# Kernel optimization log

Measured on AMD Instinct MI355X. Metric: run time of the kernel, lower is better.

Reference implementation:

```python
import jax, jax.numpy as jnp
import numpy as np

NB, B, L, D, H = 4, 4, 1024, 512, 8
E = D // H  # head dim = 64
SCALE = 1.0 / np.sqrt(E)


def setup_inputs() -> dict:
    key = jax.random.key(0)
    ks = jax.random.split(key, 18)
    w = lambda k, shape: (jax.random.normal(k, shape, dtype=jnp.float32) * 0.02)
    inp = {
        'x': jax.random.normal(ks[0], (NB, B, L, D), dtype=jnp.float32),
        # per-block intra-attention projections, stored [in, out] (x @ W + b)
        'Wq': w(ks[1], (NB, D, D)), 'bq': w(ks[2], (NB, D)),
        'Wk': w(ks[3], (NB, D, D)), 'bk': w(ks[4], (NB, D)),
        'Wv': w(ks[5], (NB, D, D)), 'bv': w(ks[6], (NB, D)),
        'Wo': w(ks[7], (NB, D, D)), 'bo': w(ks[8], (NB, D)),
        # shared inter (router) attention projections
        'iWq': w(ks[9], (D, D)), 'ibq': w(ks[10], (D,)),
        'iWk': w(ks[11], (D, D)), 'ibk': w(ks[12], (D,)),
        'iWv': w(ks[13], (D, D)), 'ibv': w(ks[14], (D,)),
        'iWo': w(ks[15], (D, D)), 'ibo': w(ks[16], (D,)),
    }
    return inp


def _full_attn(q, k, v):
    # q,k,v: [..., S, H, E] with batch dims leading; unmasked FullAttention
    scores = jnp.einsum('...lhe,...she->...hls', q, k) * SCALE
    A = jax.nn.softmax(scores, axis=-1)
    return jnp.einsum('...hls,...shd->...lhd', A, v)


def reference(x, Wq, bq, Wk, bk, Wv, bv, Wo, bo,
              iWq, ibq, iWk, ibk, iWv, ibv, iWo, ibo):
    # ---- intra attention, vectorized over the NB blocks ----
    proj = lambda W, b: (jnp.einsum('nbld,nde->nble', x, W) + b[:, None, None, :])
    q = proj(Wq, bq).reshape(NB, B, L, H, E)
    k = proj(Wk, bk).reshape(NB, B, L, H, E)
    v = proj(Wv, bv).reshape(NB, B, L, H, E)
    o = _full_attn(q, k, v).reshape(NB, B, L, D)
    x_intra = jnp.einsum('nbld,nde->nble', o, Wo) + bo[:, None, None, :]

    # ---- inter attention over router tokens (last token of each block) ----
    routers = jnp.transpose(x_intra[:, :, -1, :], (1, 0, 2))  # [B, NB, D]
    rq = (routers @ iWq + ibq).reshape(B, NB, H, E)
    rk = (routers @ iWk + ibk).reshape(B, NB, H, E)
    rv = (routers @ iWv + ibv).reshape(B, NB, H, E)
    ro = _full_attn(rq, rk, rv).reshape(B, NB, D)
    x_inter = ro @ iWo + ibo  # [B, NB, D]

    # replace each block's last (router) token with its inter-attended version
    x_out = x_intra.at[:, :, -1, :].set(jnp.transpose(x_inter, (1, 0, 2)))
    return x_out  # [NB, B, L, D]
```

## Files before the change

kernel.cpp:

```cpp
#include <hip/hip_runtime.h>
#include <math.h>

#define NBV 4
#define BBV 4
#define LLV 1024
#define DDV 512
#define HHV 8
#define EEV 64

typedef unsigned short u16;
typedef _Float16 half8 __attribute__((ext_vector_type(8)));
typedef float f32x4 __attribute__((ext_vector_type(4)));

#define QSCALE 0.1803368801111243f

__device__ __forceinline__ u16 f2h(float f) {
  union { _Float16 h; u16 u; } v; v.h = (_Float16)f; return v.u;
}
__device__ __forceinline__ unsigned pkrtz(float a, float b) {
  typedef __fp16 fp16x2 __attribute__((ext_vector_type(2)));
  union { fp16x2 h; unsigned u; } c;
  c.h = __builtin_amdgcn_cvt_pkrtz(a, b);
  return c.u;
}
__device__ __forceinline__ void gload16(const void* g, void* l) {
  __builtin_amdgcn_global_load_lds(
      (const __attribute__((address_space(1))) unsigned int*)g,
      (__attribute__((address_space(3))) unsigned int*)l, 16, 0, 0);
}

__global__ __launch_bounds__(256) void convert(
    const float* __restrict__ x,
    const float* __restrict__ Wq, const float* __restrict__ Wk,
    const float* __restrict__ Wv, const float* __restrict__ Wo,
    u16* __restrict__ x_t, u16* __restrict__ wt, u16* __restrict__ wo)
{
  const int bid = blockIdx.x;
  if (bid < 4096) {
    const int t = bid * 256 + threadIdx.x;
    const int lane = t & 63;
    const int f = (t >> 6) & 7;
    const int kt = (t >> 9) & 15;
    const int rt = t >> 13;
    const int r = rt * 128 + f * 16 + (lane & 15);
    const int k0 = kt * 32 + (lane >> 4) * 8;
    const float* s = x + (size_t)r * 512 + k0;
    float4 v0 = *(const float4*)s;
    float4 v1 = *(const float4*)(s + 4);
    float vv[8] = {v0.x, v0.y, v0.z, v0.w, v1.x, v1.y, v1.z, v1.w};
    union { u16 s16[8]; uint4 v; } H;
#pragma unroll
    for (int j = 0; j < 8; ++j) H.s16[j] = f2h(vv[j]);
    *(uint4*)(x_t + (size_t)t * 8) = H.v;
  } else {
    const int qkv = (bid < 5632);
    const int t = (qkv ? (bid - 4096) : (bid - 5632)) * 256 + threadIdx.x;
    const int z = t >> 15;
    const int tl = t & 32767;
    const int lane = tl & 63;
    const int f = (tl >> 6) & 7;
    const int kt = (tl >> 9) & 15;
    const int rt = tl >> 13;
    const float* W;
    u16* dst;
    if (qkv) {
      const int nb = z / 3, p = z - nb * 3;
      W = (p == 0 ? Wq : p == 1 ? Wk : Wv) + (size_t)nb * 262144;
      dst = wt;
    } else {
      W = Wo + (size_t)z * 262144;
      dst = wo;
    }
    const int r = rt * 128 + f * 16 + (lane & 15);
    const int k0 = kt * 32 + (lane >> 4) * 8;
    union { u16 s16[8]; uint4 v; } H;
#pragma unroll
    for (int j = 0; j < 8; ++j) H.s16[j] = f2h(W[(size_t)(k0 + j) * 512 + r]);
    *(uint4*)(dst + (size_t)z * 262144 + (size_t)tl * 8) = H.v;
  }
}

template <int MODE>
__global__ __launch_bounds__(256) void gemm_f16(
    const u16* __restrict__ Aw, const u16* __restrict__ Bx,
    const float* __restrict__ bias0, const float* __restrict__ bias1,
    const float* __restrict__ bias2,
    u16* __restrict__ q_b, u16* __restrict__ k_b, u16* __restrict__ v_t,
    float* __restrict__ Cout)
{
  __shared__ __align__(16) u16 SM[17408];
  u16* As = SM;
  u16* Bs = SM + 4096;

  const int tid = threadIdx.x;
  const int lane = tid & 63, w = tid >> 6;
  const int l15 = lane & 15, l4 = lane >> 4;
  const int bid = blockIdx.x;

  int mt, nt, z;
  if (MODE == 0) {
    const int wgid = (bid & 7) * 192 + (bid >> 3);
    mt = wgid & 3; nt = (wgid >> 2) & 31; z = wgid >> 7;
  } else {
    const int wgid = (bid & 7) * 64 + (bid >> 3);
    mt = wgid & 31; nt = (wgid >> 5) & 3; z = wgid >> 7;
  }

  int nb, p;
  const u16 *A, *B;
  if (MODE == 0) {
    nb = z / 3; p = z - nb * 3;
    A = Aw + (size_t)z * 262144;
    B = Bx + (size_t)nb * 2097152;
  } else {
    nb = z; p = 0;
    A = Aw + (size_t)z * 2097152;
    B = Bx + (size_t)z * 262144;
  }

  const f32x4 z4 = {0.f, 0.f, 0.f, 0.f};
  f32x4 acc[4][4];
#pragma unroll
  for (int i = 0; i < 4; ++i)
#pragma unroll
    for (int j = 0; j < 4; ++j) acc[i][j] = z4;

  for (int kt = 0; kt < 16; ++kt) {
    const u16* ap = A + ((size_t)(mt * 16 + kt) * 8 + w * 2) * 512 + lane * 8;
    const u16* bp = B + ((size_t)(nt * 16 + kt) * 8 + w * 2) * 512 + lane * 8;
    __syncthreads();
    gload16(ap,       As + (w * 2 + 0) * 512);
    gload16(ap + 512, As + (w * 2 + 1) * 512);
    gload16(bp,       Bs + (w * 2 + 0) * 512);
    gload16(bp + 512, Bs + (w * 2 + 1) * 512);
    __syncthreads();

    half8 a[4], b[4];
#pragma unroll
    for (int m = 0; m < 4; ++m)
      a[m] = *(const half8*)(As + ((w >> 1) * 4 + m) * 512 + lane * 8);
#pragma unroll
    for (int n = 0; n < 4; ++n)
      b[n] = *(const half8*)(Bs + ((w & 1) * 4 + n) * 512 + lane * 8);
#pragma unroll
    for (int m = 0; m < 4; ++m)
#pragma unroll
      for (int n = 0; n < 4; ++n)
        acc[m][n] = __builtin_amdgcn_mfma_f32_16x16x32_f16(a[m], b[n], acc[m][n], 0, 0, 0);
  }

  if (MODE == 0) {
    const float* bias = (p == 0 ? bias0 : p == 1 ? bias1 : bias2) + nb * 512;
    const int hh = w >> 1;
    __syncthreads();
    if (p < 2) {
      const float scl = (p == 0) ? QSCALE : 1.0f;
#pragma unroll
      for (int mm = 0; mm < 4; ++mm) {
        const int c = mm * 4 + l4;
#pragma unroll
        for (int nn = 0; nn < 4; ++nn) {
          const int tok = (w & 1) * 64 + nn * 16 + l15;
          ushort4 pk;
#pragma unroll
          for (int i = 0; i < 4; ++i) {
            const int mf = mt * 128 + hh * 64 + mm * 16 + l4 * 4 + i;
            ((u16*)&pk)[i] = f2h((acc[mm][nn][i] + bias[mf]) * scl);
          }
          *(ushort4*)((char*)SM + hh * 17408 + tok * 136 +
                      ((c ^ (tok & 15)) * 8)) = pk;
        }
      }
      __syncthreads();
      u16* dst = (p == 0 ? q_b : k_b);
#pragma unroll
      for (int i = 0; i < 16; ++i) {
        const int idx = i * 256 + tid;
        const int h2 = idx >> 11, tok = (idx >> 4) & 127, c = idx & 15;
        ushort4 v = *(const ushort4*)((char*)SM + h2 * 17408 + tok * 136 +
                                      ((c ^ (tok & 15)) * 8));
        const int ltok = nt * 128 + tok;
        const int headf = (nb * 4 + (ltok >> 10)) * 8 + mt * 2 + h2;
        *(ushort4*)(dst + (size_t)headf * 65536 + (ltok & 1023) * 64 + c * 4) = v;
      }
    } else {
#pragma unroll
      for (int mm = 0; mm < 4; ++mm) {
#pragma unroll
        for (int nn = 0; nn < 4; ++nn) {
          const int tok = (w & 1) * 64 + nn * 16 + l15;
#pragma unroll
          for (int r = 0; r < 4; ++r) {
            const int e = mm * 16 + l4 * 4 + r;
            const int mf = mt * 128 + hh * 64 + e;
            *(u16*)((char*)SM + hh * 17408 + e * 264 + tok * 2) =
                f2h(acc[mm][nn][r] + bias[mf]);
          }
        }
      }
      __syncthreads();
#pragma unroll
      for (int i = 0; i < 16; ++i) {
        const int idx = i * 256 + tid;
        const int h2 = idx >> 11, rem = idx & 2047;
        const int e = rem >> 5, s = rem & 31;
        uint2 v = *(const uint2*)((char*)SM + h2 * 17408 + e * 264 + s * 8);
        const int headf = (nb * 4 + (nt >> 3)) * 8 + mt * 2 + h2;
        *(uint2*)(v_t + (size_t)headf * 65536 + e * 1024 +
                  (nt & 7) * 128 + s * 4) = v;
      }
    }
  } else {
#pragma unroll
    for (int mm = 0; mm < 4; ++mm) {
#pragma unroll
      for (int nn = 0; nn < 4; ++nn) {
        const int m0 = mt * 128 + ((w >> 1) * 4 + mm) * 16 + l4 * 4;
        const int n  = nt * 128 + ((w & 1) * 4 + nn) * 16 + l15;
        const float bz = bias0[nb * 512 + n];
#pragma unroll
        for (int r = 0; r < 4; ++r)
          Cout[((size_t)nb * 4096 + m0 + r) * 512 + n] = acc[mm][nn][r] + bz;
      }
    }
  }
}

__global__ __launch_bounds__(512, 4) void attn_mfma(
    const u16* __restrict__ Qb, const u16* __restrict__ Kb,
    const u16* __restrict__ Vt, u16* __restrict__ o_t)
{
  __shared__ __align__(16) u16 SM[32768];
  u16* KL = SM;
  u16* VL = SM + 8192;
  u16* PL = SM + 16384;

  const int tid = threadIdx.x;
  const int lane = tid & 63, w = tid >> 6;
  const int l15 = lane & 15, l4 = lane >> 4;
  const int sb = blockIdx.x;
  const int head = sb & 127;
  const int qt = sb >> 7;
  const size_t hbase = (size_t)head * 65536;
  const int q0 = qt * 256;

  half8 qf[2][2];
#pragma unroll
  for (int qm = 0; qm < 2; ++qm) {
    const u16* qp = Qb + hbase + (size_t)(q0 + w * 32 + qm * 16 + l15) * 64 + l4 * 8;
    qf[qm][0] = *(const half8*)qp;
    qf[qm][1] = *(const half8*)(qp + 32);
  }

  const f32x4 z4 = {0.f, 0.f, 0.f, 0.f};
  const _Float16 one_h = (_Float16)1.0f;
  const half8 ones = {one_h, one_h, one_h, one_h, one_h, one_h, one_h, one_h};
  f32x4 oacc[2][4], ls[2];
#pragma unroll
  for (int qm = 0; qm < 2; ++qm) {
    ls[qm] = z4;
#pragma unroll
    for (int ef = 0; ef < 4; ++ef) oacc[qm][ef] = z4;
  }

  const int rowl = lane >> 3;
  const int colx = ((lane & 7) ^ rowl) * 8;

#define STAGE(buf, kt0)                                                        \
  {                                                                            \
    gload16(Kb + hbase + (size_t)((kt0) + w * 8 + rowl) * 64 + colx,           \
            KL + (buf) * 4096 + w * 512);                                      \
    gload16(Vt + hbase + (size_t)(w * 8 + rowl) * 1024 + (kt0) + colx,         \
            VL + (buf) * 4096 + w * 512);                                      \
  }

  STAGE(0, 0);
  __syncthreads();

  char* Pw = (char*)(PL + w * 2048);

  for (int t = 0; t < 16; ++t) {
    const int cur = t & 1;
    if (t < 15) STAGE(cur ^ 1, (t + 1) * 64);

    f32x4 st[2][4];
#pragma unroll
    for (int qm = 0; qm < 2; ++qm)
#pragma unroll
      for (int kf = 0; kf < 4; ++kf) st[qm][kf] = z4;

    __builtin_amdgcn_s_setprio(1);
#pragma unroll
    for (int kf = 0; kf < 4; ++kf) {
      const int key = kf * 16 + l15;
      const int swz = (key & 7) << 4;
#pragma unroll
      for (int eh = 0; eh < 2; ++eh) {
        half8 af = *(const half8*)((char*)(KL + cur * 4096) +
                     ((key * 128 + eh * 64 + l4 * 16) ^ swz));
        st[0][kf] = __builtin_amdgcn_mfma_f32_16x16x32_f16(af, qf[0][eh], st[0][kf], 0, 0, 0);
        st[1][kf] = __builtin_amdgcn_mfma_f32_16x16x32_f16(af, qf[1][eh], st[1][kf], 0, 0, 0);
      }
    }
    __builtin_amdgcn_s_setprio(0);

#pragma unroll
    for (int qm = 0; qm < 2; ++qm) {
      const int rq = qm * 16 + l15;
      const int rswz = (rq & 7) << 4;
#pragma unroll
      for (int kf = 0; kf < 4; ++kf) {
        float e0 = __builtin_amdgcn_exp2f(st[qm][kf][0]);
        float e1 = __builtin_amdgcn_exp2f(st[qm][kf][1]);
        float e2 = __builtin_amdgcn_exp2f(st[qm][kf][2]);
        float e3 = __builtin_amdgcn_exp2f(st[qm][kf][3]);
        uint2 d;
        d.x = pkrtz(e0, e1);
        d.y = pkrtz(e2, e3);
        *(uint2*)(Pw + ((rq * 128 + kf * 32 + l4 * 8) ^ rswz)) = d;
      }
    }

    __builtin_amdgcn_s_setprio(1);
#pragma unroll
    for (int kh = 0; kh < 2; ++kh) {
      half8 pa[2];
#pragma unroll
      for (int qm = 0; qm < 2; ++qm) {
        const int rq = qm * 16 + l15;
        pa[qm] = *(const half8*)(Pw +
                   ((rq * 128 + kh * 64 + l4 * 16) ^ ((rq & 7) << 4)));
      }
      ls[0] = __builtin_amdgcn_mfma_f32_16x16x32_f16(pa[0], ones, ls[0], 0, 0, 0);
      ls[1] = __builtin_amdgcn_mfma_f32_16x16x32_f16(pa[1], ones, ls[1], 0, 0, 0);
#pragma unroll
      for (int ef = 0; ef < 4; ++ef) {
        const int e = ef * 16 + l15;
        half8 vb2 = *(const half8*)((char*)(VL + cur * 4096) +
                      ((e * 128 + kh * 64 + l4 * 16) ^ ((e & 7) << 4)));
        oacc[0][ef] = __builtin_amdgcn_mfma_f32_16x16x32_f16(pa[0], vb2, oacc[0][ef], 0, 0, 0);
        oacc[1][ef] = __builtin_amdgcn_mfma_f32_16x16x32_f16(pa[1], vb2, oacc[1][ef], 0, 0, 0);
      }
    }
    __builtin_amdgcn_s_setprio(0);
    __syncthreads();
  }
#undef STAGE

  char* Ot = (char*)SM;
#pragma unroll
  for (int qm = 0; qm < 2; ++qm) {
    f32x4 iv;
#pragma unroll
    for (int r = 0; r < 4; ++r) iv[r] = 1.0f / ls[qm][r];
#pragma unroll
    for (int ef = 0; ef < 4; ++ef)
#pragma unroll
      for (int r = 0; r < 4; ++r) {
        const int tokl = w * 32 + qm * 16 + l4 * 4 + r;
        const int dl = ef * 16 + l15;
        *(u16*)(Ot + ((tokl * 128 + dl * 2) ^ ((tokl & 7) << 4))) =
            f2h(oacc[qm][ef][r] * iv[r]);
      }
  }
  __syncthreads();

  const int nb = head >> 5, bb = (head >> 3) & 3, h = head & 7;
  u16* abase = o_t + (size_t)nb * 2097152;
#pragma unroll
  for (int i = 0; i < 4; ++i) {
    const int gidx = i * 512 + tid;
    const int rt_loc = gidx >> 10;
    const int rem = gidx & 1023;
    const int kh = rem >> 9, f = (rem >> 6) & 7, ln = rem & 63;
    const int tokl = rt_loc * 128 + f * 16 + (ln & 15);
    const int dl = kh * 32 + (ln >> 4) * 8;
    uint4 vvv = *(const uint4*)(Ot + ((tokl * 128 + dl * 2) ^ ((tokl & 7) << 4)));
    const int rt = bb * 8 + qt * 2 + rt_loc;
    *(uint4*)(abase + ((size_t)((rt * 16 + h * 2 + kh) * 8 + f) * 512 + ln * 8)) = vvv;
  }
}

__global__ __launch_bounds__(256) void inter_qkv(
    const float* __restrict__ xout,
    const float* __restrict__ iWq, const float* __restrict__ iWk, const float* __restrict__ iWv,
    const float* __restrict__ ibq, const float* __restrict__ ibk, const float* __restrict__ ibv,
    float* __restrict__ rq, float* __restrict__ rk, float* __restrict__ rv)
{
    __shared__ float Rs[16][512];
    __shared__ float P[16][68];
    const int tid = threadIdx.x;
    for (int t = tid; t < 2048; t += 256) {
        const int row = t >> 7, k4 = (t & 127) * 4;
        const int n = row & 3, b = row >> 2;
        *(float4*)&Rs[row][k4] =
            *(const float4*)&xout[(((size_t)(n * BBV + b) * LLV) + (LLV - 1)) * DDV + k4];
    }
    __syncthreads();

    const int which = blockIdx.y;
    const float* W    = which == 0 ? iWq : which == 1 ? iWk : iWv;
    const float* bias = which == 0 ? ibq : which == 1 ? ibk : ibv;
    float*       out  = which == 0 ? rq  : which == 1 ? rk  : rv;

    const int cb = blockIdx.x * 64;
    const int c4 = (tid & 15) * 4;
    const int kq = tid >> 4;

    f32x4 acc[16];
#pragma unroll
    for (int r = 0; r < 16; ++r) acc[r] = (f32x4){0.f, 0.f, 0.f, 0.f};

    for (int i = 0; i < 32; ++i) {
        const int k = i * 16 + kq;
        const float4 wv = *(const float4*)&W[(size_t)k * 512 + cb + c4];
#pragma unroll
        for (int r = 0; r < 16; ++r) {
            const float rv_ = Rs[r][k];
            acc[r][0] += rv_ * wv.x;
            acc[r][1] += rv_ * wv.y;
            acc[r][2] += rv_ * wv.z;
            acc[r][3] += rv_ * wv.w;
        }
    }

#pragma unroll
    for (int r = 0; r < 16; ++r) {
        *(f32x4*)&P[kq][c4] = acc[r];
        __syncthreads();
        if (tid < 64) {
            float s = 0.f;
#pragma unroll
            for (int q = 0; q < 16; ++q) s += P[q][tid];
            out[(size_t)r * 512 + cb + tid] = s + bias[cb + tid];
        }
        __syncthreads();
    }
}

__global__ __launch_bounds__(64) void inter_attn(
    const float* __restrict__ rq, const float* __restrict__ rk,
    const float* __restrict__ rv, float* __restrict__ ro)
{
    const int b = blockIdx.x >> 3, h = blockIdx.x & 7;
    const int e = threadIdx.x;
    float qv[4], kv[4], vv[4];
#pragma unroll
    for (int n = 0; n < 4; ++n) {
        const size_t base = (size_t)(b * 4 + n) * 512 + h * 64 + e;
        qv[n] = rq[base]; kv[n] = rk[base]; vv[n] = rv[base];
    }
    float s[4][4];
#pragma unroll
    for (int n = 0; n < 4; ++n)
#pragma unroll
        for (int m = 0; m < 4; ++m) {
            float prod = qv[n] * kv[m];
#pragma unroll
            for (int off = 1; off < 64; off <<= 1) prod += __shfl_xor(prod, off);
            s[n][m] = prod * 0.125f;
        }
#pragma unroll
    for (int n = 0; n < 4; ++n) {
        float mx = fmaxf(fmaxf(s[n][0], s[n][1]), fmaxf(s[n][2], s[n][3]));
        float pr[4], den = 0.f, ov = 0.f;
#pragma unroll
        for (int m = 0; m < 4; ++m) { pr[m] = __expf(s[n][m] - mx); den += pr[m]; }
#pragma unroll
        for (int m = 0; m < 4; ++m) ov += pr[m] * vv[m];
        ro[(size_t)(b * 4 + n) * 512 + h * 64 + e] = ov / den;
    }
}

__global__ __launch_bounds__(256) void inter_out(
    const float* __restrict__ ro, const float* __restrict__ iWo,
    const float* __restrict__ ibo, float* __restrict__ out)
{
    __shared__ float Rs[16][512];
    __shared__ float P[16][68];
    const int tid = threadIdx.x;
    for (int t = tid; t < 2048; t += 256)
        *(float4*)&Rs[t >> 7][(t & 127) * 4] = *(const float4*)&ro[t * 4];
    __syncthreads();

    const int cb = blockIdx.x * 64;
    const int c4 = (tid & 15) * 4;
    const int kq = tid >> 4;

    f32x4 acc[16];
#pragma unroll
    for (int r = 0; r < 16; ++r) acc[r] = (f32x4){0.f, 0.f, 0.f, 0.f};

    for (int i = 0; i < 32; ++i) {
        const int k = i * 16 + kq;
        const float4 wv = *(const float4*)&iWo[(size_t)k * 512 + cb + c4];
#pragma unroll
        for (int r = 0; r < 16; ++r) {
            const float rv_ = Rs[r][k];
            acc[r][0] += rv_ * wv.x;
            acc[r][1] += rv_ * wv.y;
            acc[r][2] += rv_ * wv.z;
            acc[r][3] += rv_ * wv.w;
        }
    }

#pragma unroll
    for (int r = 0; r < 16; ++r) {
        *(f32x4*)&P[kq][c4] = acc[r];
        __syncthreads();
        if (tid < 64) {
            float s = 0.f;
#pragma unroll
            for (int q = 0; q < 16; ++q) s += P[q][tid];
            const int b = r >> 2, n = r & 3;
            out[(((size_t)(n * BBV + b) * LLV) + (LLV - 1)) * DDV + cb + tid] =
                s + ibo[cb + tid];
        }
        __syncthreads();
    }
}

extern "C" void kernel_launch(void* const* d_in, const int* in_sizes, int n_in,
                              void* d_out, int out_size, void* d_ws, size_t ws_size,
                              hipStream_t stream)
{
    (void)in_sizes; (void)n_in; (void)out_size; (void)ws_size;
    const float* x   = (const float*)d_in[0];
    const float* Wq  = (const float*)d_in[1];  const float* bq  = (const float*)d_in[2];
    const float* Wk  = (const float*)d_in[3];  const float* bk  = (const float*)d_in[4];
    const float* Wv  = (const float*)d_in[5];  const float* bv  = (const float*)d_in[6];
    const float* Wo  = (const float*)d_in[7];  const float* bo  = (const float*)d_in[8];
    const float* iWq = (const float*)d_in[9];  const float* ibq = (const float*)d_in[10];
    const float* iWk = (const float*)d_in[11]; const float* ibk = (const float*)d_in[12];
    const float* iWv = (const float*)d_in[13]; const float* ibv = (const float*)d_in[14];
    const float* iWo = (const float*)d_in[15]; const float* ibo = (const float*)d_in[16];
    float* out = (float*)d_out;

    char* W = (char*)d_ws;
    u16* x_t  = (u16*)(W);
    u16* wt   = (u16*)(W + 16777216);
    u16* wo   = (u16*)(W + 33554432);
    u16* q_b  = (u16*)(W + 35651584);
    u16* k_b  = (u16*)(W + 52428800);
    u16* v_t  = (u16*)(W + 69206016);
    u16* o_t  = (u16*)(W + 85983232);
    float* rq = (float*)(W + 102760448);
    float* rk = rq + 8192;
    float* rv = rk + 8192;
    float* ro = rv + 8192;

    convert<<<6144, 256, 0, stream>>>(x, Wq, Wk, Wv, Wo, x_t, wt, wo);
    gemm_f16<0><<<1536, 256, 0, stream>>>(
        wt, x_t, bq, bk, bv, q_b, k_b, v_t, nullptr);
    attn_mfma<<<512, 512, 0, stream>>>(q_b, k_b, v_t, o_t);
    gemm_f16<1><<<512, 256, 0, stream>>>(
        o_t, wo, bo, nullptr, nullptr, nullptr, nullptr, nullptr, out);
    inter_qkv<<<dim3(8, 3), 256, 0, stream>>>(out, iWq, iWk, iWv, ibq, ibk, ibv, rq, rk, rv);
    inter_attn<<<32, 64, 0, stream>>>(rq, rk, rv, ro);
    inter_out<<<8, 256, 0, stream>>>(ro, iWo, ibo, out);
}
```

Measured before the change: 149.1 us.

## Shrink attention P buffer to raise occupancy and fuse inter QKV with inter attention

The attention kernel now computes exp and writes P in two half-tiles, one per kh, into a smaller padded per-wave buffer (80-byte rows instead of 128-byte swizzled rows). This cuts shared memory from 64KB to 52KB and raises the launch-bounds occupancy hint from 4 to 6. Separately, the inter-router QKV projection and the 4-token inter attention are fused into one 32-block kernel, which removes a launch and the rq/rk/rv round trip through global memory. The trade-offs are possible LDS bank conflicts from the unswizzled padded P layout, tighter register limits at the higher occupancy, and less parallelism in the fused inter kernel.

```diff
diff --git a/kernel.cpp b/kernel.cpp
--- a/kernel.cpp
+++ b/kernel.cpp
@@ -226,11 +226,11 @@
   }
 }
 
-__global__ __launch_bounds__(512, 4) void attn_mfma(
+__global__ __launch_bounds__(512, 6) void attn_mfma(
     const u16* __restrict__ Qb, const u16* __restrict__ Kb,
     const u16* __restrict__ Vt, u16* __restrict__ o_t)
 {
-  __shared__ __align__(16) u16 SM[32768];
+  __shared__ __align__(16) u16 SM[26624];
   u16* KL = SM;
   u16* VL = SM + 8192;
   u16* PL = SM + 16384;
@@ -277,7 +277,7 @@
   STAGE(0, 0);
   __syncthreads();
 
-  char* Pw = (char*)(PL + w * 2048);
+  char* Pw = (char*)(PL + w * 1280);
 
   for (int t = 0; t < 16; ++t) {
     const int cur = t & 1;
@@ -305,44 +305,38 @@
     __builtin_amdgcn_s_setprio(0);
 
 #pragma unroll
-    for (int qm = 0; qm < 2; ++qm) {
-      const int rq = qm * 16 + l15;
-      const int rswz = (rq & 7) << 4;
-#pragma unroll
-      for (int kf = 0; kf < 4; ++kf) {
-        float e0 = __builtin_amdgcn_exp2f(st[qm][kf][0]);
-        float e1 = __builtin_amdgcn_exp2f(st[qm][kf][1]);
-        float e2 = __builtin_amdgcn_exp2f(st[qm][kf][2]);
-        float e3 = __builtin_amdgcn_exp2f(st[qm][kf][3]);
-        uint2 d;
-        d.x = pkrtz(e0, e1);
-        d.y = pkrtz(e2, e3);
-        *(uint2*)(Pw + ((rq * 128 + kf * 32 + l4 * 8) ^ rswz)) = d;
-      }
-    }
-
-    __builtin_amdgcn_s_setprio(1);
-#pragma unroll
     for (int kh = 0; kh < 2; ++kh) {
-      half8 pa[2];
 #pragma unroll
       for (int qm = 0; qm < 2; ++qm) {
-        const int rq = qm * 16 + l15;
-        pa[qm] = *(const half8*)(Pw +
-                   ((rq * 128 + kh * 64 + l4 * 16) ^ ((rq & 7) << 4)));
-      }
-      ls[0] = __builtin_amdgcn_mfma_f32_16x16x32_f16(pa[0], ones, ls[0], 0, 0, 0);
-      ls[1] = __builtin_amdgcn_mfma_f32_16x16x32_f16(pa[1], ones, ls[1], 0, 0, 0);
+        const int row = qm * 16 + l15;
+#pragma unroll
+        for (int kf2 = 0; kf2 < 2; ++kf2) {
+          const int kf = kh * 2 + kf2;
+          float e0 = __builtin_amdgcn_exp2f(st[qm][kf][0]);
+          float e1 = __builtin_amdgcn_exp2f(st[qm][kf][1]);
+          float e2 = __builtin_amdgcn_exp2f(st[qm][kf][2]);
+          float e3 = __builtin_amdgcn_exp2f(st[qm][kf][3]);
+          uint2 d;
+          d.x = pkrtz(e0, e1);
+          d.y = pkrtz(e2, e3);
+          *(uint2*)(Pw + row * 80 + kf2 * 32 + l4 * 8) = d;
+        }
+      }
+      __builtin_amdgcn_s_setprio(1);
+      half8 pa0 = *(const half8*)(Pw + l15 * 80 + l4 * 16);
+      half8 pa1 = *(const half8*)(Pw + (16 + l15) * 80 + l4 * 16);
+      ls[0] = __builtin_amdgcn_mfma_f32_16x16x32_f16(pa0, ones, ls[0], 0, 0, 0);
+      ls[1] = __builtin_amdgcn_mfma_f32_16x16x32_f16(pa1, ones, ls[1], 0, 0, 0);
 #pragma unroll
       for (int ef = 0; ef < 4; ++ef) {
         const int e = ef * 16 + l15;
         half8 vb2 = *(const half8*)((char*)(VL + cur * 4096) +
                       ((e * 128 + kh * 64 + l4 * 16) ^ ((e & 7) << 4)));
-        oacc[0][ef] = __builtin_amdgcn_mfma_f32_16x16x32_f16(pa[0], vb2, oacc[0][ef], 0, 0, 0);
-        oacc[1][ef] = __builtin_amdgcn_mfma_f32_16x16x32_f16(pa[1], vb2, oacc[1][ef], 0, 0, 0);
-      }
-    }
-    __builtin_amdgcn_s_setprio(0);
+        oacc[0][ef] = __builtin_amdgcn_mfma_f32_16x16x32_f16(pa0, vb2, oacc[0][ef], 0, 0, 0);
+        oacc[1][ef] = __builtin_amdgcn_mfma_f32_16x16x32_f16(pa1, vb2, oacc[1][ef], 0, 0, 0);
+      }
+      __builtin_amdgcn_s_setprio(0);
+    }
     __syncthreads();
   }
 #undef STAGE
@@ -381,94 +375,91 @@
   }
 }
 
-__global__ __launch_bounds__(256) void inter_qkv(
+__global__ __launch_bounds__(256) void inter_qa(
     const float* __restrict__ xout,
     const float* __restrict__ iWq, const float* __restrict__ iWk, const float* __restrict__ iWv,
     const float* __restrict__ ibq, const float* __restrict__ ibk, const float* __restrict__ ibv,
-    float* __restrict__ rq, float* __restrict__ rk, float* __restrict__ rv)
+    float* __restrict__ ro)
 {
-    __shared__ float Rs[16][512];
-    __shared__ float P[16][68];
+    __shared__ float Rs[4][512];
+    __shared__ float Pp[4][12][64];
+    __shared__ float R2[3][4][64];
     const int tid = threadIdx.x;
-    for (int t = tid; t < 2048; t += 256) {
-        const int row = t >> 7, k4 = (t & 127) * 4;
-        const int n = row & 3, b = row >> 2;
-        *(float4*)&Rs[row][k4] =
+    const int b = blockIdx.x >> 3, h = blockIdx.x & 7;
+
+    for (int t = tid; t < 512; t += 256) {
+        const int n = t >> 7, k4 = (t & 127) * 4;
+        *(float4*)&Rs[n][k4] =
             *(const float4*)&xout[(((size_t)(n * BBV + b) * LLV) + (LLV - 1)) * DDV + k4];
     }
     __syncthreads();
 
-    const int which = blockIdx.y;
-    const float* W    = which == 0 ? iWq : which == 1 ? iWk : iWv;
-    const float* bias = which == 0 ? ibq : which == 1 ? ibk : ibv;
-    float*       out  = which == 0 ? rq  : which == 1 ? rk  : rv;
-
-    const int cb = blockIdx.x * 64;
-    const int c4 = (tid & 15) * 4;
-    const int kq = tid >> 4;
-
-    f32x4 acc[16];
-#pragma unroll
-    for (int r = 0; r < 16; ++r) acc[r] = (f32x4){0.f, 0.f, 0.f, 0.f};
-
-    for (int i = 0; i < 32; ++i) {
-        const int k = i * 16 + kq;
-        const float4 wv = *(const float4*)&W[(size_t)k * 512 + cb + c4];
-#pragma unroll
-        for (int r = 0; r < 16; ++r) {
-            const float rv_ = Rs[r][k];
-            acc[r][0] += rv_ * wv.x;
-            acc[r][1] += rv_ * wv.y;
-            acc[r][2] += rv_ * wv.z;
-            acc[r][3] += rv_ * wv.w;
-        }
-    }
-
-#pragma unroll
-    for (int r = 0; r < 16; ++r) {
-        *(f32x4*)&P[kq][c4] = acc[r];
-        __syncthreads();
-        if (tid < 64) {
-            float s = 0.f;
-#pragma unroll
-            for (int q = 0; q < 16; ++q) s += P[q][tid];
-            out[(size_t)r * 512 + cb + tid] = s + bias[cb + tid];
-        }
-        __syncthreads();
-    }
-}
-
-__global__ __launch_bounds__(64) void inter_attn(
-    const float* __restrict__ rq, const float* __restrict__ rk,
-    const float* __restrict__ rv, float* __restrict__ ro)
-{
-    const int b = blockIdx.x >> 3, h = blockIdx.x & 7;
-    const int e = threadIdx.x;
-    float qv[4], kv[4], vv[4];
-#pragma unroll
-    for (int n = 0; n < 4; ++n) {
-        const size_t base = (size_t)(b * 4 + n) * 512 + h * 64 + e;
-        qv[n] = rq[base]; kv[n] = rk[base]; vv[n] = rv[base];
-    }
-    float s[4][4];
-#pragma unroll
-    for (int n = 0; n < 4; ++n)
-#pragma unroll
-        for (int m = 0; m < 4; ++m) {
-            float prod = qv[n] * kv[m];
-#pragma unroll
-            for (int off = 1; off < 64; off <<= 1) prod += __shfl_xor(prod, off);
-            s[n][m] = prod * 0.125f;
-        }
-#pragma unroll
-    for (int n = 0; n < 4; ++n) {
-        float mx = fmaxf(fmaxf(s[n][0], s[n][1]), fmaxf(s[n][2], s[n][3]));
-        float pr[4], den = 0.f, ov = 0.f;
-#pragma unroll
-        for (int m = 0; m < 4; ++m) { pr[m] = __expf(s[n][m] - mx); den += pr[m]; }
-#pragma unroll
-        for (int m = 0; m < 4; ++m) ov += pr[m] * vv[m];
-        ro[(size_t)(b * 4 + n) * 512 + h * 64 + e] = ov / den;
+    const int g = tid >> 6;
+    const int e = tid & 63;
+    const int col = h * 64 + e;
+    float acc[3][4];
+#pragma unroll
+    for (int p = 0; p < 3; ++p)
+#pragma unroll
+        for (int n = 0; n < 4; ++n) acc[p][n] = 0.f;
+
+#pragma unroll 2
+    for (int kk = 0; kk < 128; ++kk) {
+        const int k = g * 128 + kk;
+        const float wq = iWq[(size_t)k * 512 + col];
+        const float wk = iWk[(size_t)k * 512 + col];
+        const float wv = iWv[(size_t)k * 512 + col];
+#pragma unroll
+        for (int n = 0; n < 4; ++n) {
+            const float rv_ = Rs[n][k];
+            acc[0][n] += rv_ * wq;
+            acc[1][n] += rv_ * wk;
+            acc[2][n] += rv_ * wv;
+        }
+    }
+#pragma unroll
+    for (int p = 0; p < 3; ++p)
+#pragma unroll
+        for (int n = 0; n < 4; ++n)
+            Pp[g][p * 4 + n][e] = acc[p][n];
+    __syncthreads();
+
+#pragma unroll
+    for (int p = 0; p < 3; ++p) {
+        const int n = g;
+        float s = Pp[0][p * 4 + n][e] + Pp[1][p * 4 + n][e] +
+                  Pp[2][p * 4 + n][e] + Pp[3][p * 4 + n][e];
+        const float* bias = (p == 0 ? ibq : p == 1 ? ibk : ibv);
+        R2[p][n][e] = s + bias[col];
+    }
+    __syncthreads();
+
+    if (tid < 64) {
+        float qv[4], kv[4], vv[4];
+#pragma unroll
+        for (int n = 0; n < 4; ++n) {
+            qv[n] = R2[0][n][tid]; kv[n] = R2[1][n][tid]; vv[n] = R2[2][n][tid];
+        }
+        float s[4][4];
+#pragma unroll
+        for (int n = 0; n < 4; ++n)
+#pragma unroll
+            for (int m = 0; m < 4; ++m) {
+                float prod = qv[n] * kv[m];
+#pragma unroll
+                for (int off = 1; off < 64; off <<= 1) prod += __shfl_xor(prod, off);
+                s[n][m] = prod * 0.125f;
+            }
+#pragma unroll
+        for (int n = 0; n < 4; ++n) {
+            float mx = fmaxf(fmaxf(s[n][0], s[n][1]), fmaxf(s[n][2], s[n][3]));
+            float pr[4], den = 0.f, ov = 0.f;
+#pragma unroll
+            for (int m = 0; m < 4; ++m) { pr[m] = __expf(s[n][m] - mx); den += pr[m]; }
+#pragma unroll
+            for (int m = 0; m < 4; ++m) ov += pr[m] * vv[m];
+            ro[(size_t)(b * 4 + n) * 512 + h * 64 + tid] = ov / den;
+        }
     }
 }
 
@@ -544,10 +535,7 @@
     u16* k_b  = (u16*)(W + 52428800);
     u16* v_t  = (u16*)(W + 69206016);
     u16* o_t  = (u16*)(W + 85983232);
-    float* rq = (float*)(W + 102760448);
-    float* rk = rq + 8192;
-    float* rv = rk + 8192;
-    float* ro = rv + 8192;
+    float* ro = (float*)(W + 102760448);
 
     convert<<<6144, 256, 0, stream>>>(x, Wq, Wk, Wv, Wo, x_t, wt, wo);
     gemm_f16<0><<<1536, 256, 0, stream>>>(
@@ -555,7 +543,6 @@
     attn_mfma<<<512, 512, 0, stream>>>(q_b, k_b, v_t, o_t);
     gemm_f16<1><<<512, 256, 0, stream>>>(
         o_t, wo, bo, nullptr, nullptr, nullptr, nullptr, nullptr, out);
-    inter_qkv<<<dim3(8, 3), 256, 0, stream>>>(out, iWq, iWk, iWv, ibq, ibk, ibv, rq, rk, rv);
-    inter_attn<<<32, 64, 0, stream>>>(rq, rk, rv, ro);
+    inter_qa<<<32, 256, 0, stream>>>(out, iWq, iWk, iWv, ibq, ibk, ibv, ro);
     inter_out<<<8, 256, 0, stream>>>(ro, iWo, ibo, out);
 }
```

Result: slower. 341.0 us (+128.6%).

## Triple-buffer attention K/V with explicit vmcnt waits and double K-step GEMM tiles

Applied to the files above, without the earlier changes.

The attention kernel moves from a double-buffered to a triple-buffered K/V pipeline. It uses hand-placed s_waitcnt vmcnt and s_barrier so two tiles stay in flight while the current one is computed. The P tile is split into halves with a padded 80-byte row stride instead of XOR swizzle, which interleaves exp with the PV MFMAs and shrinks the per-wave P buffer. The projection GEMM now loads two K-steps per barrier pair, halving synchronisation count at the cost of more LDS. The risks are more LDS per block, which may lower occupancy, and fragile hand-counted vmcnt values.

```diff
diff --git a/kernel.cpp b/kernel.cpp
--- a/kernel.cpp
+++ b/kernel.cpp
@@ -90,7 +90,7 @@
 {
   __shared__ __align__(16) u16 SM[17408];
   u16* As = SM;
-  u16* Bs = SM + 4096;
+  u16* Bs = SM + 8192;
 
   const int tid = threadIdx.x;
   const int lane = tid & 63, w = tid >> 6;
@@ -125,28 +125,34 @@
 #pragma unroll
     for (int j = 0; j < 4; ++j) acc[i][j] = z4;
 
-  for (int kt = 0; kt < 16; ++kt) {
-    const u16* ap = A + ((size_t)(mt * 16 + kt) * 8 + w * 2) * 512 + lane * 8;
-    const u16* bp = B + ((size_t)(nt * 16 + kt) * 8 + w * 2) * 512 + lane * 8;
+  for (int kt = 0; kt < 8; ++kt) {
     __syncthreads();
-    gload16(ap,       As + (w * 2 + 0) * 512);
-    gload16(ap + 512, As + (w * 2 + 1) * 512);
-    gload16(bp,       Bs + (w * 2 + 0) * 512);
-    gload16(bp + 512, Bs + (w * 2 + 1) * 512);
+#pragma unroll
+    for (int s = 0; s < 2; ++s) {
+      const u16* ap = A + ((size_t)((mt * 16 + kt * 2 + s) * 8) + w * 2) * 512 + lane * 8;
+      const u16* bp = B + ((size_t)((nt * 16 + kt * 2 + s) * 8) + w * 2) * 512 + lane * 8;
+      gload16(ap,       As + (s * 8 + w * 2 + 0) * 512);
+      gload16(ap + 512, As + (s * 8 + w * 2 + 1) * 512);
+      gload16(bp,       Bs + (s * 8 + w * 2 + 0) * 512);
+      gload16(bp + 512, Bs + (s * 8 + w * 2 + 1) * 512);
+    }
     __syncthreads();
 
-    half8 a[4], b[4];
-#pragma unroll
-    for (int m = 0; m < 4; ++m)
-      a[m] = *(const half8*)(As + ((w >> 1) * 4 + m) * 512 + lane * 8);
-#pragma unroll
-    for (int n = 0; n < 4; ++n)
-      b[n] = *(const half8*)(Bs + ((w & 1) * 4 + n) * 512 + lane * 8);
-#pragma unroll
-    for (int m = 0; m < 4; ++m)
+#pragma unroll
+    for (int s = 0; s < 2; ++s) {
+      half8 a[4], b[4];
+#pragma unroll
+      for (int m = 0; m < 4; ++m)
+        a[m] = *(const half8*)(As + (s * 8 + (w >> 1) * 4 + m) * 512 + lane * 8);
 #pragma unroll
       for (int n = 0; n < 4; ++n)
-        acc[m][n] = __builtin_amdgcn_mfma_f32_16x16x32_f16(a[m], b[n], acc[m][n], 0, 0, 0);
+        b[n] = *(const half8*)(Bs + (s * 8 + (w & 1) * 4 + n) * 512 + lane * 8);
+#pragma unroll
+      for (int m = 0; m < 4; ++m)
+#pragma unroll
+        for (int n = 0; n < 4; ++n)
+          acc[m][n] = __builtin_amdgcn_mfma_f32_16x16x32_f16(a[m], b[n], acc[m][n], 0, 0, 0);
+    }
   }
 
   if (MODE == 0) {
@@ -230,10 +236,10 @@
     const u16* __restrict__ Qb, const u16* __restrict__ Kb,
     const u16* __restrict__ Vt, u16* __restrict__ o_t)
 {
-  __shared__ __align__(16) u16 SM[32768];
+  __shared__ __align__(16) u16 SM[34816];
   u16* KL = SM;
-  u16* VL = SM + 8192;
-  u16* PL = SM + 16384;
+  u16* VL = SM + 12288;
+  u16* PL = SM + 24576;
 
   const int tid = threadIdx.x;
   const int lane = tid & 63, w = tid >> 6;
@@ -244,14 +250,6 @@
   const size_t hbase = (size_t)head * 65536;
   const int q0 = qt * 256;
 
-  half8 qf[2][2];
-#pragma unroll
-  for (int qm = 0; qm < 2; ++qm) {
-    const u16* qp = Qb + hbase + (size_t)(q0 + w * 32 + qm * 16 + l15) * 64 + l4 * 8;
-    qf[qm][0] = *(const half8*)qp;
-    qf[qm][1] = *(const half8*)(qp + 32);
-  }
-
   const f32x4 z4 = {0.f, 0.f, 0.f, 0.f};
   const _Float16 one_h = (_Float16)1.0f;
   const half8 ones = {one_h, one_h, one_h, one_h, one_h, one_h, one_h, one_h};
@@ -274,14 +272,28 @@
             VL + (buf) * 4096 + w * 512);                                      \
   }
 
+  half8 qf[2][2];
+#pragma unroll
+  for (int qm = 0; qm < 2; ++qm) {
+    const u16* qp = Qb + hbase + (size_t)(q0 + w * 32 + qm * 16 + l15) * 64 + l4 * 8;
+    qf[qm][0] = *(const half8*)qp;
+    qf[qm][1] = *(const half8*)(qp + 32);
+  }
+
   STAGE(0, 0);
-  __syncthreads();
-
-  char* Pw = (char*)(PL + w * 2048);
+  STAGE(1, 64);
+  STAGE(2, 128);
+
+  char* Pw = (char*)(PL + w * 1280);
 
   for (int t = 0; t < 16; ++t) {
-    const int cur = t & 1;
-    if (t < 15) STAGE(cur ^ 1, (t + 1) * 64);
+    const int cur = t % 3;
+    if (t <= 13)      { asm volatile("s_waitcnt vmcnt(4)" ::: "memory"); }
+    else if (t == 14) { asm volatile("s_waitcnt vmcnt(2)" ::: "memory"); }
+    else              { asm volatile("s_waitcnt vmcnt(0)" ::: "memory"); }
+    __builtin_amdgcn_sched_barrier(0);
+    __builtin_amdgcn_s_barrier();
+    __builtin_amdgcn_sched_barrier(0);
 
     f32x4 st[2][4];
 #pragma unroll
@@ -305,45 +317,44 @@
     __builtin_amdgcn_s_setprio(0);
 
 #pragma unroll
-    for (int qm = 0; qm < 2; ++qm) {
-      const int rq = qm * 16 + l15;
-      const int rswz = (rq & 7) << 4;
-#pragma unroll
-      for (int kf = 0; kf < 4; ++kf) {
-        float e0 = __builtin_amdgcn_exp2f(st[qm][kf][0]);
-        float e1 = __builtin_amdgcn_exp2f(st[qm][kf][1]);
-        float e2 = __builtin_amdgcn_exp2f(st[qm][kf][2]);
-        float e3 = __builtin_amdgcn_exp2f(st[qm][kf][3]);
-        uint2 d;
-        d.x = pkrtz(e0, e1);
-        d.y = pkrtz(e2, e3);
-        *(uint2*)(Pw + ((rq * 128 + kf * 32 + l4 * 8) ^ rswz)) = d;
-      }
-    }
-
-    __builtin_amdgcn_s_setprio(1);
-#pragma unroll
     for (int kh = 0; kh < 2; ++kh) {
-      half8 pa[2];
 #pragma unroll
       for (int qm = 0; qm < 2; ++qm) {
-        const int rq = qm * 16 + l15;
-        pa[qm] = *(const half8*)(Pw +
-                   ((rq * 128 + kh * 64 + l4 * 16) ^ ((rq & 7) << 4)));
-      }
-      ls[0] = __builtin_amdgcn_mfma_f32_16x16x32_f16(pa[0], ones, ls[0], 0, 0, 0);
-      ls[1] = __builtin_amdgcn_mfma_f32_16x16x32_f16(pa[1], ones, ls[1], 0, 0, 0);
+        const int row = qm * 16 + l15;
+#pragma unroll
+        for (int kf2 = 0; kf2 < 2; ++kf2) {
+          const int kf = kh * 2 + kf2;
+          float e0 = __builtin_amdgcn_exp2f(st[qm][kf][0]);
+          float e1 = __builtin_amdgcn_exp2f(st[qm][kf][1]);
+          float e2 = __builtin_amdgcn_exp2f(st[qm][kf][2]);
+          float e3 = __builtin_amdgcn_exp2f(st[qm][kf][3]);
+          uint2 d;
+          d.x = pkrtz(e0, e1);
+          d.y = pkrtz(e2, e3);
+          *(uint2*)(Pw + row * 80 + kf2 * 32 + l4 * 8) = d;
+        }
+      }
+      __builtin_amdgcn_s_setprio(1);
+      half8 pa0 = *(const half8*)(Pw + l15 * 80 + l4 * 16);
+      half8 pa1 = *(const half8*)(Pw + (16 + l15) * 80 + l4 * 16);
+      ls[0] = __builtin_amdgcn_mfma_f32_16x16x32_f16(pa0, ones, ls[0], 0, 0, 0);
+      ls[1] = __builtin_amdgcn_mfma_f32_16x16x32_f16(pa1, ones, ls[1], 0, 0, 0);
 #pragma unroll
       for (int ef = 0; ef < 4; ++ef) {
         const int e = ef * 16 + l15;
         half8 vb2 = *(const half8*)((char*)(VL + cur * 4096) +
                       ((e * 128 + kh * 64 + l4 * 16) ^ ((e & 7) << 4)));
-        oacc[0][ef] = __builtin_amdgcn_mfma_f32_16x16x32_f16(pa[0], vb2, oacc[0][ef], 0, 0, 0);
-        oacc[1][ef] = __builtin_amdgcn_mfma_f32_16x16x32_f16(pa[1], vb2, oacc[1][ef], 0, 0, 0);
-      }
-    }
-    __builtin_amdgcn_s_setprio(0);
-    __syncthreads();
+        oacc[0][ef] = __builtin_amdgcn_mfma_f32_16x16x32_f16(pa0, vb2, oacc[0][ef], 0, 0, 0);
+        oacc[1][ef] = __builtin_amdgcn_mfma_f32_16x16x32_f16(pa1, vb2, oacc[1][ef], 0, 0, 0);
+      }
+      __builtin_amdgcn_s_setprio(0);
+    }
+
+    asm volatile("s_waitcnt lgkmcnt(0)" ::: "memory");
+    __builtin_amdgcn_sched_barrier(0);
+    __builtin_amdgcn_s_barrier();
+    __builtin_amdgcn_sched_barrier(0);
+    if (t < 13) STAGE(cur, (t + 3) * 64);
   }
 #undef STAGE
 
```

Result: faster. 145.8 us (-2.2%).
